# Kernel tuning notes

Measured on AMD Instinct MI355X. Metric: run time of the kernel, lower is better.

The kernel has to match this reference:

```python
import jax, jax.numpy as jnp
import numpy as np

B, T, F, H = 512, 365, 16, 256


def _lstm_layer(x, W_ih, W_hh, b_ih, b_hh):
    """batch_first LSTM layer, torch gate order (i, f, g, o).
    x: [B, T, in]. Returns (outputs [B, T, H], final h [B, H])."""
    # Precompute input projections for all timesteps: [T, B, 4H]
    x_proj = jnp.einsum('bti,gi->tbg', x, W_ih) + (b_ih + b_hh)
    h0 = jnp.zeros((x.shape[0], W_hh.shape[1]), x.dtype)
    c0 = jnp.zeros_like(h0)

    def step(carry, xp):
        h, c = carry
        z = xp + h @ W_hh.T  # [B, 4H]
        i, f, g, o = jnp.split(z, 4, axis=-1)
        c = jax.nn.sigmoid(f) * c + jax.nn.sigmoid(i) * jnp.tanh(g)
        h = jax.nn.sigmoid(o) * jnp.tanh(c)
        return (h, c), h

    (hT, _), hs = jax.lax.scan(step, (h0, c0), x_proj)
    return jnp.transpose(hs, (1, 0, 2)), hT


def setup_inputs() -> dict:
    key = jax.random.key(0)
    ks = jax.random.split(key, 11)
    s1 = 1.0 / np.sqrt(H)
    u = lambda k, shape: jax.random.uniform(k, shape, jnp.float32, -s1, s1)
    return {
        'x': jax.random.normal(ks[0], (B, T, F), jnp.float32),
        'W_ih1': u(ks[1], (4 * H, F)),
        'W_hh1': u(ks[2], (4 * H, H)),
        'b_ih1': u(ks[3], (4 * H,)),
        'b_hh1': u(ks[4], (4 * H,)),
        'W_ih2': u(ks[5], (4 * H, H)),
        'W_hh2': u(ks[6], (4 * H, H)),
        'b_ih2': u(ks[7], (4 * H,)),
        'b_hh2': u(ks[8], (4 * H,)),
        'W_lin': u(ks[9], (1, H)),
        'b_lin': u(ks[10], (1,)),
    }


def reference(x, W_ih1, W_hh1, b_ih1, b_hh1, W_ih2, W_hh2, b_ih2, b_hh2, W_lin, b_lin):
    h1_seq, _ = _lstm_layer(x, W_ih1, W_hh1, b_ih1, b_hh1)
    # dropout(p=0.1) is identity in eval mode
    _, hT = _lstm_layer(h1_seq, W_ih2, W_hh2, b_ih2, b_hh2)
    out = (hT @ W_lin.T + b_lin).reshape(-1)  # [B]
    return out
```

## Files before the change

### kernel.cpp

```cpp
#include <hip/hip_runtime.h>


#define T_STEPS 365
#define RS 564

typedef __attribute__((ext_vector_type(8))) short short8;
typedef __attribute__((ext_vector_type(4))) float float4_;
typedef __attribute__((ext_vector_type(4))) unsigned int uint4_;
typedef unsigned long long u64;
typedef unsigned int u32;

#define MFMA16(a, b, c) __builtin_amdgcn_mfma_f32_16x16x32_bf16((a), (b), (c), 0, 0, 0)

__device__ __forceinline__ unsigned short f2bf(float v) {
    union { float f; u32 u; } a; a.f = v;
    u32 r = a.u + 0x7fffu + ((a.u >> 16) & 1u);
    return (unsigned short)(r >> 16);
}
__device__ __forceinline__ float bf2f(unsigned short h) {
    union { u32 u; float f; } a; a.u = ((u32)h) << 16; return a.f;
}
__device__ __forceinline__ u32 packhl(float v) {
    unsigned short hi = f2bf(v);
    unsigned short lo = f2bf(v - bf2f(hi));
    return ((u32)hi << 16) | (u32)lo;
}
__device__ __forceinline__ float sigm(float x)  { return 1.f / (1.f + __expf(-x)); }
__device__ __forceinline__ float tanh_(float x) { return 2.f / (1.f + __expf(-2.f * x)) - 1.f; }

__device__ __forceinline__ void unpk(uint4_ a, uint4_ b, short8& hi, short8& lo) {
    union U { u32 d[4]; short8 s; } H, L;
    H.d[0] = __builtin_amdgcn_perm(a.y, a.x, 0x07060302u);
    H.d[1] = __builtin_amdgcn_perm(a.w, a.z, 0x07060302u);
    H.d[2] = __builtin_amdgcn_perm(b.y, b.x, 0x07060302u);
    H.d[3] = __builtin_amdgcn_perm(b.w, b.z, 0x07060302u);
    L.d[0] = __builtin_amdgcn_perm(a.y, a.x, 0x05040100u);
    L.d[1] = __builtin_amdgcn_perm(a.w, a.z, 0x05040100u);
    L.d[2] = __builtin_amdgcn_perm(b.y, b.x, 0x05040100u);
    L.d[3] = __builtin_amdgcn_perm(b.w, b.z, 0x05040100u);
    hi = H.s; lo = L.s;
}

__global__ void prep_w(
    const float* __restrict__ Wih1, const float* __restrict__ Whh1,
    const float* __restrict__ bih1, const float* __restrict__ bhh1,
    const float* __restrict__ Wih2, const float* __restrict__ Whh2,
    const float* __restrict__ bih2, const float* __restrict__ bhh2,
    unsigned short* __restrict__ w1h, unsigned short* __restrict__ w1l,
    unsigned short* __restrict__ w2h, unsigned short* __restrict__ w2l,
    float* __restrict__ bias1, float* __restrict__ bias2)
{
    const int tile = blockIdx.x;
    const int g = tile >> 4, ns = tile & 15;
    const int tid = threadIdx.x;

    for (int idx = tid; idx < 9 * 512; idx += 256) {
        int ks = idx >> 9, off = idx & 511, r = off >> 5, kk = off & 31;
        int R = g * 256 + ns * 16 + r;
        float v;
        if (ks < 8)       v = Whh1[R * 256 + ks * 32 + kk];
        else if (kk < 16) v = Wih1[R * 16 + kk];
        else              v = 0.f;
        unsigned short h = f2bf(v);
        size_t d = (size_t)(tile * 9 + ks) * 512 + off;
        w1h[d] = h; w1l[d] = f2bf(v - bf2f(h));
    }
    for (int idx = tid; idx < 16 * 512; idx += 256) {
        int ks = idx >> 9, off = idx & 511, r = off >> 5, kk = off & 31;
        int R = g * 256 + ns * 16 + r;
        int k = ks * 32 + kk;
        float v = (k < 256) ? Wih2[R * 256 + k] : Whh2[R * 256 + (k - 256)];
        unsigned short h = f2bf(v);
        size_t d = (size_t)(tile * 16 + ks) * 512 + off;
        w2h[d] = h; w2l[d] = f2bf(v - bf2f(h));
    }
    if (tid < 16) {
        int R = g * 256 + ns * 16 + tid;
        bias1[R] = bih1[R] + bhh1[R];
        bias2[R] = bih2[R] + bhh2[R];
    }
}

__global__ __launch_bounds__(512, 2) void lstm_main(
    const float* __restrict__ x,
    const unsigned short* __restrict__ w1h, const unsigned short* __restrict__ w1l,
    const unsigned short* __restrict__ w2h, const unsigned short* __restrict__ w2l,
    const float* __restrict__ bias1, const float* __restrict__ bias2,
    u32* hb1, u32* hb2, u32* prog,
    const float* __restrict__ Wlin, const float* __restrict__ blin,
    float* __restrict__ out)
{
    __shared__ __align__(16) u32 A2u[32 * RS];
    __shared__ __align__(16) float zb1[3 * 64 * 36];
    __shared__ __align__(16) float zb2[5 * 64 * 36];
    __shared__ __align__(16) float hp[32][17];

    const int tid  = threadIdx.x;
    const int lane = tid & 63;
    const int wv   = tid >> 6;
    const int quad = lane >> 4;
    const int r16  = lane & 15;
    const int bg   = blockIdx.x & 15;
    const int ns   = blockIdx.x >> 4;

    u32* myprog = prog + bg * 64;

    const bool isL1 = (wv < 3);
    int t0, t1_, t2_, t3_;
    if      (wv == 0) { t0 = 0;  t1_ = 1;  t2_ = 2;  t3_ = -1; }
    else if (wv == 1) { t0 = 3;  t1_ = 4;  t2_ = 5;  t3_ = -1; }
    else if (wv == 2) { t0 = 6;  t1_ = 7;  t2_ = 8;  t3_ = -1; }
    else if (wv == 3) { t0 = 0;  t1_ = 1;  t2_ = 2;  t3_ = 3;  }
    else if (wv == 4) { t0 = 4;  t1_ = 5;  t2_ = 6;  t3_ = -1; }
    else if (wv == 5) { t0 = 7;  t1_ = 9;  t2_ = 10; t3_ = -1; }
    else if (wv == 6) { t0 = 11; t1_ = 12; t2_ = 13; t3_ = -1; }
    else              { t0 = 14; t1_ = 15; t2_ = 16; t3_ = -1; }

    const int loff = r16 * 32 + quad * 8;
    const unsigned short* WHsrc = isL1 ? w1h : w2h;
    const unsigned short* WLsrc = isL1 ? w1l : w2l;
    const int NK = isL1 ? 9 : 16;
    short8 WH[4][4], WL[4][4];
#pragma unroll
    for (int s = 0; s < 4; s++) {
        const int b = (s == 0) ? t0 : (s == 1) ? t1_ : (s == 2) ? t2_ : t3_;
#pragma unroll
        for (int g = 0; g < 4; g++) {
            if (b >= 0) {
                int ks = (!isL1 && b > 8) ? (b - 1) : b;
                size_t off = ((size_t)((g * 16 + ns) * NK + ks)) * 512 + loff;
                WH[g][s] = *(const short8*)(WHsrc + off);
                WL[g][s] = *(const short8*)(WLsrc + off);
            } else {
                WH[g][s] = short8{0,0,0,0,0,0,0,0};
                WL[g][s] = short8{0,0,0,0,0,0,0,0};
            }
        }
    }

    float bi[4] = {0.f, 0.f, 0.f, 0.f};
    if (tid < 256) {
        const float* bsrc = (tid < 128) ? bias1 : bias2;
        int colg = ns * 16 + (tid & 15);
#pragma unroll
        for (int g = 0; g < 4; g++) bi[g] = bsrc[g * 256 + colg];
    }
    float cst[4] = {0.f, 0.f, 0.f, 0.f};

    for (int i = tid; i < 32 * RS; i += 512) A2u[i] = 0u;
    __syncthreads();
    {
        int row = tid >> 4, col = tid & 15;
        float v = x[((size_t)(bg * 32 + row) * T_STEPS + 0) * 16 + col];
        A2u[row * RS + 256 + col] = packhl(v);
    }
    __syncthreads();

    for (int t = 0; t <= T_STEPS; t++) {
        const int p = t & 1;

        float4_ acc[4][2];
        const float4_ z4 = {0.f, 0.f, 0.f, 0.f};
#pragma unroll
        for (int g = 0; g < 4; g++) { acc[g][0] = z4; acc[g][1] = z4; }

#pragma unroll
        for (int s = 0; s < 4; s++) {
            const int b = (s == 0) ? t0 : (s == 1) ? t1_ : (s == 2) ? t2_ : t3_;
            if (b >= 0) {
                const int base0 = r16 * RS + b * 32 + quad * 8;
                uint4_ p00 = *(const uint4_*)&A2u[base0];
                uint4_ p01 = *(const uint4_*)&A2u[base0 + 4];
                uint4_ p10 = *(const uint4_*)&A2u[base0 + 16 * RS];
                uint4_ p11 = *(const uint4_*)&A2u[base0 + 16 * RS + 4];
                short8 ah0, al0, ah1, al1;
                unpk(p00, p01, ah0, al0);
                unpk(p10, p11, ah1, al1);
#pragma unroll
                for (int g = 0; g < 4; g++) {
                    acc[g][0] = MFMA16(ah0, WH[g][s], acc[g][0]);
                    acc[g][0] = MFMA16(al0, WH[g][s], acc[g][0]);
                    acc[g][0] = MFMA16(ah0, WL[g][s], acc[g][0]);
                    acc[g][1] = MFMA16(ah1, WH[g][s], acc[g][1]);
                    acc[g][1] = MFMA16(al1, WH[g][s], acc[g][1]);
                    acc[g][1] = MFMA16(ah1, WL[g][s], acc[g][1]);
                }
            }
        }
        {
            float* zbase = isL1 ? (zb1 + wv * (64 * 36)) : (zb2 + (wv - 3) * (64 * 36));
#pragma unroll
            for (int g = 0; g < 4; g++)
#pragma unroll
                for (int rt = 0; rt < 2; rt++)
                    *(float4_*)&zbase[(size_t)(g * 16 + r16) * 36 + rt * 16 + quad * 4] = acc[g][rt];
        }
        __syncthreads();

        if (tid < 256) {
            const bool is1 = (tid < 128);
            const int hcol = tid & 15;
            const int rq   = (tid >> 4) & 7;
            const float* zb = is1 ? zb1 : zb2;
            const int np = is1 ? 3 : 5;
            float4_ z[4];
#pragma unroll
            for (int g = 0; g < 4; g++) {
                float4_ s = {bi[g], bi[g], bi[g], bi[g]};
#pragma unroll
                for (int pw = 0; pw < 5; pw++) {
                    if (pw < np)
                        s += *(const float4_*)&zb[(size_t)(pw * 64 + g * 16 + hcol) * 36 + rq * 4];
                }
                z[g] = s;
            }
            u32* hb = is1 ? hb1 : hb2;
            const int slot = is1 ? p : (1 - p);
            size_t o = (((size_t)slot * 16 + bg) * 32 + rq * 4) * 256 + ns * 16 + hcol;
#pragma unroll
            for (int j = 0; j < 4; j++) {
                float zi = z[0][j], zf = z[1][j], zg = z[2][j], zo = z[3][j];
                float nc = sigm(zf) * cst[j] + sigm(zi) * tanh_(zg);
                float h  = sigm(zo) * tanh_(nc);
                if (!is1 && t == 0) { nc = 0.f; h = 0.f; }
                cst[j] = nc;
                __hip_atomic_store(&hb[o + (size_t)j * 256], packhl(h),
                                   __ATOMIC_RELAXED, __HIP_MEMORY_SCOPE_WORKGROUP);
            }
            asm volatile("s_waitcnt vmcnt(0)" ::: "memory");
            if (lane == 0)
                __hip_atomic_store(&myprog[ns * 4 + wv], (u32)(t + 1),
                                   __ATOMIC_RELAXED, __HIP_MEMORY_SCOPE_WORKGROUP);
        } else {
            const int i0 = tid - 256;
            const int tn = (t + 1 <= T_STEPS - 1) ? (t + 1) : (T_STEPS - 1);
#pragma unroll
            for (int k = 0; k < 2; k++) {
                int idx = i0 + 256 * k;
                int row = idx >> 4, col = idx & 15;
                float v = x[((size_t)(bg * 32 + row) * T_STEPS + tn) * 16 + col];
                A2u[row * RS + 256 + col] = packhl(v);
            }
        }

        if (t == T_STEPS) break;

        {
            const u32 tgt = (u32)(t + 1);
            while (__hip_atomic_load(&myprog[lane], __ATOMIC_RELAXED,
                                     __HIP_MEMORY_SCOPE_AGENT) < tgt)
                __builtin_amdgcn_s_sleep(1);
        }

        {
            const u64* s1 = (const u64*)(hb1 + (size_t)(p * 16 + bg) * 32 * 256);
            const u64* s2 = (const u64*)(hb2 + (size_t)((1 - p) * 16 + bg) * 32 * 256);
#pragma unroll
            for (int j = 0; j < 4; j++) {
                const int row = wv * 4 + j;
                const u64* r1 = s1 + (size_t)row * 128;
                const u64* r2 = s2 + (size_t)row * 128;
                u64 a = __hip_atomic_load(r1 + lane,      __ATOMIC_RELAXED, __HIP_MEMORY_SCOPE_AGENT);
                u64 b = __hip_atomic_load(r1 + 64 + lane, __ATOMIC_RELAXED, __HIP_MEMORY_SCOPE_AGENT);
                u64 c = __hip_atomic_load(r2 + lane,      __ATOMIC_RELAXED, __HIP_MEMORY_SCOPE_AGENT);
                u64 d = __hip_atomic_load(r2 + 64 + lane, __ATOMIC_RELAXED, __HIP_MEMORY_SCOPE_AGENT);
                u32* dst = &A2u[row * RS];
                *(u64*)&dst[2 * lane]             = a;
                *(u64*)&dst[128 + 2 * lane]       = b;
                *(u64*)&dst[288 + 2 * lane]       = c;
                *(u64*)&dst[288 + 128 + 2 * lane] = d;
            }
        }
        __syncthreads();
    }

    if (ns != 0) return;
    {
        const u32 tgt = (u32)(T_STEPS + 1);
        while (__hip_atomic_load(&myprog[lane], __ATOMIC_RELAXED,
                                 __HIP_MEMORY_SCOPE_AGENT) < tgt)
            __builtin_amdgcn_s_sleep(1);
    }
    {
        int row = tid >> 4, seg = tid & 15;
        const u32* src = hb2 + ((size_t)bg * 32 + row) * 256 + seg * 16;
        float s = 0.f;
#pragma unroll
        for (int j = 0; j < 16; j++) {
            u32 v = __hip_atomic_load(&src[j], __ATOMIC_RELAXED, __HIP_MEMORY_SCOPE_AGENT);
            s += (bf2f((unsigned short)(v >> 16)) + bf2f((unsigned short)v)) * Wlin[seg * 16 + j];
        }
        hp[row][seg] = s;
    }
    __syncthreads();
    if (tid < 32) {
        float s = 0.f;
#pragma unroll
        for (int j = 0; j < 16; j++) s += hp[tid][j];
        out[bg * 32 + tid] = s + blin[0];
    }
}

extern "C" void kernel_launch(void* const* d_in, const int* in_sizes, int n_in,
                              void* d_out, int out_size, void* d_ws, size_t ws_size,
                              hipStream_t stream) {
    const float* x    = (const float*)d_in[0];
    const float* Wih1 = (const float*)d_in[1];
    const float* Whh1 = (const float*)d_in[2];
    const float* bih1 = (const float*)d_in[3];
    const float* bhh1 = (const float*)d_in[4];
    const float* Wih2 = (const float*)d_in[5];
    const float* Whh2 = (const float*)d_in[6];
    const float* bih2 = (const float*)d_in[7];
    const float* bhh2 = (const float*)d_in[8];
    const float* Wlin = (const float*)d_in[9];
    const float* blin = (const float*)d_in[10];
    float* out = (float*)d_out;

    char* pp = (char*)d_ws;
    unsigned short* w1h = (unsigned short*)pp; pp += (size_t)64 * 9 * 512 * 2;
    unsigned short* w1l = (unsigned short*)pp; pp += (size_t)64 * 9 * 512 * 2;
    unsigned short* w2h = (unsigned short*)pp; pp += (size_t)64 * 16 * 512 * 2;
    unsigned short* w2l = (unsigned short*)pp; pp += (size_t)64 * 16 * 512 * 2;
    float* bias1 = (float*)pp; pp += 1024 * 4;
    float* bias2 = (float*)pp; pp += 1024 * 4;
    char* zero_base = pp;
    u32* hb1 = (u32*)pp; pp += (size_t)2 * 16 * 32 * 256 * 4;
    u32* hb2 = (u32*)pp; pp += (size_t)2 * 16 * 32 * 256 * 4;
    u32* prog = (u32*)pp; pp += 16 * 64 * 4;
    size_t zero_bytes = (size_t)(pp - zero_base);

    hipMemsetAsync(zero_base, 0, zero_bytes, stream);
    prep_w<<<64, 256, 0, stream>>>(Wih1, Whh1, bih1, bhh1, Wih2, Whh2, bih2, bhh2,
                                   w1h, w1l, w2h, w2l, bias1, bias2);
    lstm_main<<<256, 512, 0, stream>>>(x, w1h, w1l, w2h, w2l, bias1, bias2,
                                       hb1, hb2, prog, Wlin, blin, out);
}
```

Measured before the change: 1.654 ms.

## Load recurrent hidden state directly from global into MFMA operands with prefetch

Drops the per-step staging of both layers' hidden states through a large LDS buffer. Each wave now loads its own K-slices straight from global memory into registers, double-buffered so the next slice is fetched while MFMAs run on the current one. The global h layout is rearranged so these loads match the MFMA operand layout. Only the small x input stays in LDS, and the progress wait moves to the top of each step. The cost is more global traffic per wave, since each wave fetches its slices on its own and some slices are read by several blocks, and latency is exposed if the prefetch does not cover it.

After: 1.812 ms. 1.1x slower.

```diff
diff --git a/kernel.cpp b/kernel.cpp
--- a/kernel.cpp
+++ b/kernel.cpp
@@ -2,7 +2,7 @@
 
 
 #define T_STEPS 365
-#define RS 564
+#define XSTR 36
 
 typedef __attribute__((ext_vector_type(8))) short short8;
 typedef __attribute__((ext_vector_type(4))) float float4_;
@@ -11,6 +11,7 @@
 typedef unsigned int u32;
 
 #define MFMA16(a, b, c) __builtin_amdgcn_mfma_f32_16x16x32_bf16((a), (b), (c), 0, 0, 0)
+#define LD64(p) __hip_atomic_load((p), __ATOMIC_RELAXED, __HIP_MEMORY_SCOPE_AGENT)
 
 __device__ __forceinline__ unsigned short f2bf(float v) {
     union { float f; u32 u; } a; a.f = v;
@@ -81,6 +82,7 @@
     }
 }
 
+
 __global__ __launch_bounds__(512, 2) void lstm_main(
     const float* __restrict__ x,
     const unsigned short* __restrict__ w1h, const unsigned short* __restrict__ w1l,
@@ -90,7 +92,7 @@
     const float* __restrict__ Wlin, const float* __restrict__ blin,
     float* __restrict__ out)
 {
-    __shared__ __align__(16) u32 A2u[32 * RS];
+    __shared__ __align__(16) u32 xbuf[32 * XSTR];
     __shared__ __align__(16) float zb1[3 * 64 * 36];
     __shared__ __align__(16) float zb2[5 * 64 * 36];
     __shared__ __align__(16) float hp[32][17];
@@ -106,15 +108,15 @@
     u32* myprog = prog + bg * 64;
 
     const bool isL1 = (wv < 3);
-    int t0, t1_, t2_, t3_;
-    if      (wv == 0) { t0 = 0;  t1_ = 1;  t2_ = 2;  t3_ = -1; }
-    else if (wv == 1) { t0 = 3;  t1_ = 4;  t2_ = 5;  t3_ = -1; }
-    else if (wv == 2) { t0 = 6;  t1_ = 7;  t2_ = 8;  t3_ = -1; }
-    else if (wv == 3) { t0 = 0;  t1_ = 1;  t2_ = 2;  t3_ = 3;  }
-    else if (wv == 4) { t0 = 4;  t1_ = 5;  t2_ = 6;  t3_ = -1; }
-    else if (wv == 5) { t0 = 7;  t1_ = 9;  t2_ = 10; t3_ = -1; }
-    else if (wv == 6) { t0 = 11; t1_ = 12; t2_ = 13; t3_ = -1; }
-    else              { t0 = 14; t1_ = 15; t2_ = 16; t3_ = -1; }
+    int s0, s1, s2, s3;
+    if      (wv == 0) { s0 = 0;  s1 = 1;  s2 = 2;  s3 = -1; }
+    else if (wv == 1) { s0 = 3;  s1 = 4;  s2 = 5;  s3 = -1; }
+    else if (wv == 2) { s0 = 6;  s1 = 7;  s2 = 8;  s3 = -1; }
+    else if (wv == 3) { s0 = 0;  s1 = 1;  s2 = 2;  s3 = 3;  }
+    else if (wv == 4) { s0 = 4;  s1 = 5;  s2 = 6;  s3 = -1; }
+    else if (wv == 5) { s0 = 7;  s1 = 8;  s2 = 9;  s3 = -1; }
+    else if (wv == 6) { s0 = 10; s1 = 11; s2 = 12; s3 = -1; }
+    else              { s0 = 13; s1 = 14; s2 = 15; s3 = -1; }
 
     const int loff = r16 * 32 + quad * 8;
     const unsigned short* WHsrc = isL1 ? w1h : w2h;
@@ -123,12 +125,11 @@
     short8 WH[4][4], WL[4][4];
 #pragma unroll
     for (int s = 0; s < 4; s++) {
-        const int b = (s == 0) ? t0 : (s == 1) ? t1_ : (s == 2) ? t2_ : t3_;
+        const int b = (s == 0) ? s0 : (s == 1) ? s1 : (s == 2) ? s2 : s3;
 #pragma unroll
         for (int g = 0; g < 4; g++) {
             if (b >= 0) {
-                int ks = (!isL1 && b > 8) ? (b - 1) : b;
-                size_t off = ((size_t)((g * 16 + ns) * NK + ks)) * 512 + loff;
+                size_t off = ((size_t)((g * 16 + ns) * NK + b)) * 512 + loff;
                 WH[g][s] = *(const short8*)(WHsrc + off);
                 WL[g][s] = *(const short8*)(WLsrc + off);
             } else {
@@ -147,46 +148,82 @@
     }
     float cst[4] = {0.f, 0.f, 0.f, 0.f};
 
-    for (int i = tid; i < 32 * RS; i += 512) A2u[i] = 0u;
+    for (int i = tid; i < 32 * XSTR; i += 512) xbuf[i] = 0u;
     __syncthreads();
     {
         int row = tid >> 4, col = tid & 15;
         float v = x[((size_t)(bg * 32 + row) * T_STEPS + 0) * 16 + col];
-        A2u[row * RS + 256 + col] = packhl(v);
+        xbuf[row * XSTR + col] = packhl(v);
     }
     __syncthreads();
+
+#define ISSUE(Fv, sid) do {                                                   \
+        if ((sid) >= 0 && !(isL1 && (sid) == 8)) {                            \
+            const u64* bp_ = (isL1 || (sid) < 8) ? h1base : h2base;           \
+            int kb_ = (isL1 || (sid) < 8) ? (sid) : ((sid) - 8);              \
+            const u64* a_ = bp_ + (size_t)kb_ * 512 + (size_t)quad * 128      \
+                                + (size_t)r16 * 2;                            \
+            Fv[0] = LD64(a_ + 0);  Fv[1] = LD64(a_ + 1);                      \
+            Fv[2] = LD64(a_ + 64); Fv[3] = LD64(a_ + 65);                     \
+            Fv[4] = LD64(a_ + 32); Fv[5] = LD64(a_ + 33);                     \
+            Fv[6] = LD64(a_ + 96); Fv[7] = LD64(a_ + 97);                     \
+        } } while (0)
+
+#define PROC(Fv, sid, sreg) do {                                              \
+        if ((sid) >= 0) {                                                     \
+            uint4_ q00, q01, q10, q11;                                        \
+            if (isL1 && (sid) == 8) {                                         \
+                q00 = *(const uint4_*)&xbuf[r16 * XSTR + quad * 8];           \
+                q01 = *(const uint4_*)&xbuf[r16 * XSTR + quad * 8 + 4];       \
+                q10 = *(const uint4_*)&xbuf[(16 + r16) * XSTR + quad * 8];    \
+                q11 = *(const uint4_*)&xbuf[(16 + r16) * XSTR + quad * 8 + 4];\
+            } else {                                                          \
+                union { u64 q[2]; uint4_ v; } u0_, u1_, u2_, u3_;             \
+                u0_.q[0] = Fv[0]; u0_.q[1] = Fv[1]; q00 = u0_.v;              \
+                u1_.q[0] = Fv[2]; u1_.q[1] = Fv[3]; q01 = u1_.v;              \
+                u2_.q[0] = Fv[4]; u2_.q[1] = Fv[5]; q10 = u2_.v;              \
+                u3_.q[0] = Fv[6]; u3_.q[1] = Fv[7]; q11 = u3_.v;              \
+            }                                                                 \
+            short8 ah0, al0, ah1, al1;                                        \
+            unpk(q00, q01, ah0, al0);                                         \
+            unpk(q10, q11, ah1, al1);                                         \
+            _Pragma("unroll")                                                 \
+            for (int g = 0; g < 4; g++) {                                     \
+                acc[g][0] = MFMA16(ah0, WH[g][sreg], acc[g][0]);              \
+                acc[g][0] = MFMA16(al0, WH[g][sreg], acc[g][0]);              \
+                acc[g][0] = MFMA16(ah0, WL[g][sreg], acc[g][0]);              \
+                acc[g][1] = MFMA16(ah1, WH[g][sreg], acc[g][1]);              \
+                acc[g][1] = MFMA16(al1, WH[g][sreg], acc[g][1]);              \
+                acc[g][1] = MFMA16(ah1, WL[g][sreg], acc[g][1]);              \
+            }                                                                 \
+        } } while (0)
 
     for (int t = 0; t <= T_STEPS; t++) {
         const int p = t & 1;
 
+        {
+            const u32 tgt = (u32)t;
+            while (__hip_atomic_load(&myprog[lane], __ATOMIC_RELAXED,
+                                     __HIP_MEMORY_SCOPE_AGENT) < tgt)
+                __builtin_amdgcn_s_sleep(1);
+        }
+        __syncthreads();
+
+        const u64* h1base = (const u64*)hb1 + (size_t)((1 - p) * 16 + bg) * 4096;
+        const u64* h2base = (const u64*)hb2 + (size_t)(p * 16 + bg) * 4096;
+
         float4_ acc[4][2];
         const float4_ z4 = {0.f, 0.f, 0.f, 0.f};
 #pragma unroll
         for (int g = 0; g < 4; g++) { acc[g][0] = z4; acc[g][1] = z4; }
 
-#pragma unroll
-        for (int s = 0; s < 4; s++) {
-            const int b = (s == 0) ? t0 : (s == 1) ? t1_ : (s == 2) ? t2_ : t3_;
-            if (b >= 0) {
-                const int base0 = r16 * RS + b * 32 + quad * 8;
-                uint4_ p00 = *(const uint4_*)&A2u[base0];
-                uint4_ p01 = *(const uint4_*)&A2u[base0 + 4];
-                uint4_ p10 = *(const uint4_*)&A2u[base0 + 16 * RS];
-                uint4_ p11 = *(const uint4_*)&A2u[base0 + 16 * RS + 4];
-                short8 ah0, al0, ah1, al1;
-                unpk(p00, p01, ah0, al0);
-                unpk(p10, p11, ah1, al1);
-#pragma unroll
-                for (int g = 0; g < 4; g++) {
-                    acc[g][0] = MFMA16(ah0, WH[g][s], acc[g][0]);
-                    acc[g][0] = MFMA16(al0, WH[g][s], acc[g][0]);
-                    acc[g][0] = MFMA16(ah0, WL[g][s], acc[g][0]);
-                    acc[g][1] = MFMA16(ah1, WH[g][s], acc[g][1]);
-                    acc[g][1] = MFMA16(al1, WH[g][s], acc[g][1]);
-                    acc[g][1] = MFMA16(ah1, WL[g][s], acc[g][1]);
-                }
-            }
-        }
+        u64 F0[8], F1[8];
+        ISSUE(F0, s0); ISSUE(F1, s1);
+        PROC(F0, s0, 0); ISSUE(F0, s2);
+        PROC(F1, s1, 1); ISSUE(F1, s3);
+        PROC(F0, s2, 2);
+        PROC(F1, s3, 3);
+
         {
             float* zbase = isL1 ? (zb1 + wv * (64 * 36)) : (zb2 + (wv - 3) * (64 * 36));
 #pragma unroll
@@ -216,7 +253,10 @@
             }
             u32* hb = is1 ? hb1 : hb2;
             const int slot = is1 ? p : (1 - p);
-            size_t o = (((size_t)slot * 16 + bg) * 32 + rq * 4) * 256 + ns * 16 + hcol;
+            const int gc = ns * 16 + hcol;
+            const size_t ob = (size_t)(slot * 16 + bg) * 8192
+                            + (gc >> 5) * 1024 + ((gc >> 3) & 3) * 256
+                            + ((gc >> 2) & 1) * 128 + rq * 16 + (gc & 3);
 #pragma unroll
             for (int j = 0; j < 4; j++) {
                 float zi = z[0][j], zf = z[1][j], zg = z[2][j], zo = z[3][j];
@@ -224,7 +264,7 @@
                 float h  = sigm(zo) * tanh_(nc);
                 if (!is1 && t == 0) { nc = 0.f; h = 0.f; }
                 cst[j] = nc;
-                __hip_atomic_store(&hb[o + (size_t)j * 256], packhl(h),
+                __hip_atomic_store(&hb[ob + (size_t)j * 4], packhl(h),
                                    __ATOMIC_RELAXED, __HIP_MEMORY_SCOPE_WORKGROUP);
             }
             asm volatile("s_waitcnt vmcnt(0)" ::: "memory");
@@ -239,39 +279,9 @@
                 int idx = i0 + 256 * k;
                 int row = idx >> 4, col = idx & 15;
                 float v = x[((size_t)(bg * 32 + row) * T_STEPS + tn) * 16 + col];
-                A2u[row * RS + 256 + col] = packhl(v);
+                xbuf[row * XSTR + col] = packhl(v);
             }
         }
-
-        if (t == T_STEPS) break;
-
-        {
-            const u32 tgt = (u32)(t + 1);
-            while (__hip_atomic_load(&myprog[lane], __ATOMIC_RELAXED,
-                                     __HIP_MEMORY_SCOPE_AGENT) < tgt)
-                __builtin_amdgcn_s_sleep(1);
-        }
-
-        {
-            const u64* s1 = (const u64*)(hb1 + (size_t)(p * 16 + bg) * 32 * 256);
-            const u64* s2 = (const u64*)(hb2 + (size_t)((1 - p) * 16 + bg) * 32 * 256);
-#pragma unroll
-            for (int j = 0; j < 4; j++) {
-                const int row = wv * 4 + j;
-                const u64* r1 = s1 + (size_t)row * 128;
-                const u64* r2 = s2 + (size_t)row * 128;
-                u64 a = __hip_atomic_load(r1 + lane,      __ATOMIC_RELAXED, __HIP_MEMORY_SCOPE_AGENT);
-                u64 b = __hip_atomic_load(r1 + 64 + lane, __ATOMIC_RELAXED, __HIP_MEMORY_SCOPE_AGENT);
-                u64 c = __hip_atomic_load(r2 + lane,      __ATOMIC_RELAXED, __HIP_MEMORY_SCOPE_AGENT);
-                u64 d = __hip_atomic_load(r2 + 64 + lane, __ATOMIC_RELAXED, __HIP_MEMORY_SCOPE_AGENT);
-                u32* dst = &A2u[row * RS];
-                *(u64*)&dst[2 * lane]             = a;
-                *(u64*)&dst[128 + 2 * lane]       = b;
-                *(u64*)&dst[288 + 2 * lane]       = c;
-                *(u64*)&dst[288 + 128 + 2 * lane] = d;
-            }
-        }
-        __syncthreads();
     }
 
     if (ns != 0) return;
@@ -283,11 +293,14 @@
     }
     {
         int row = tid >> 4, seg = tid & 15;
-        const u32* src = hb2 + ((size_t)bg * 32 + row) * 256 + seg * 16;
+        const size_t sb = (size_t)(0 * 16 + bg) * 8192;
         float s = 0.f;
 #pragma unroll
         for (int j = 0; j < 16; j++) {
-            u32 v = __hip_atomic_load(&src[j], __ATOMIC_RELAXED, __HIP_MEMORY_SCOPE_AGENT);
+            int gc = seg * 16 + j;
+            size_t idx = sb + (gc >> 5) * 1024 + ((gc >> 3) & 3) * 256
+                       + ((gc >> 2) & 1) * 128 + row * 4 + (gc & 3);
+            u32 v = __hip_atomic_load(&hb2[idx], __ATOMIC_RELAXED, __HIP_MEMORY_SCOPE_AGENT);
             s += (bf2f((unsigned short)(v >> 16)) + bf2f((unsigned short)v)) * Wlin[seg * 16 + j];
         }
         hp[row][seg] = s;
@@ -325,8 +338,8 @@
     float* bias1 = (float*)pp; pp += 1024 * 4;
     float* bias2 = (float*)pp; pp += 1024 * 4;
     char* zero_base = pp;
-    u32* hb1 = (u32*)pp; pp += (size_t)2 * 16 * 32 * 256 * 4;
-    u32* hb2 = (u32*)pp; pp += (size_t)2 * 16 * 32 * 256 * 4;
+    u32* hb1 = (u32*)pp; pp += (size_t)2 * 16 * 8192 * 4;
+    u32* hb2 = (u32*)pp; pp += (size_t)2 * 16 * 8192 * 4;
     u32* prog = (u32*)pp; pp += 16 * 64 * 4;
     size_t zero_bytes = (size_t)(pp - zero_base);
 
```
